# Kernel tuning notes

Hardware: AMD Instinct MI355X
Metric: run time of the kernel (lower is better)

## Reference

```python
import jax, jax.numpy as jnp
import numpy as np

NUM_HEADS = 16
DIM = 1024

def setup_inputs() -> dict:
    key = jax.random.key(0)
    ks = jax.random.split(key, 12)
    B, N, T, C = 4, 4096, 77, DIM
    s = 1.0 / np.sqrt(C)
    return {
        "hidden_states": jax.random.normal(ks[0], (B, N, C), jnp.float32),
        "encoder_hidden_states": jax.random.normal(ks[1], (B, T, C), jnp.float32),
        "attention_mask": jnp.zeros((B, N, T), jnp.float32),
        "Wq": jax.random.normal(ks[2], (C, C), jnp.float32) * s,
        "bq": jnp.zeros((C,), jnp.float32),
        "Wk": jax.random.normal(ks[3], (C, C), jnp.float32) * s,
        "bk": jnp.zeros((C,), jnp.float32),
        "Wv": jax.random.normal(ks[4], (C, C), jnp.float32) * s,
        "bv": jnp.zeros((C,), jnp.float32),
        "Wo": jax.random.normal(ks[5], (C, C), jnp.float32) * s,
        "bo": jnp.zeros((C,), jnp.float32),
    }

def reference(hidden_states, encoder_hidden_states, attention_mask,
              Wq, bq, Wk, bk, Wv, bv, Wo, bo):
    B, N, C = hidden_states.shape
    T = encoder_hidden_states.shape[1]
    H = NUM_HEADS
    D = C // H
    # QKV projections (torch Linear: x @ W.T + b)
    q = (hidden_states @ Wq.T + bq).reshape(B, N, H, D).transpose(0, 2, 1, 3)   # bhnd
    k = (encoder_hidden_states @ Wk.T + bk).reshape(B, T, H, D).transpose(0, 2, 1, 3)  # bhtd
    v = (encoder_hidden_states @ Wv.T + bv).reshape(B, T, H, D).transpose(0, 2, 1, 3)  # bhtd
    scale = 1.0 / jnp.sqrt(jnp.asarray(D, q.dtype))
    # scores [B,H,N,T]; additive mask broadcast over heads
    scores = jnp.einsum('bhnd,bhtd->bhnt', q, k) * scale + attention_mask[:, None, :, :]
    attn = jax.nn.softmax(scores, axis=-1)
    out = jnp.einsum('bhnt,bhtd->bhnd', attn, v)
    out = out.transpose(0, 2, 1, 3).reshape(B, N, C)
    return out @ Wo.T + bo
```

## Files before the change

### kernel.cpp

```cpp
#include <hip/hip_runtime.h>
#include <cstdint>

typedef __bf16 bf16x8 __attribute__((ext_vector_type(8)));
typedef float f32x4 __attribute__((ext_vector_type(4)));
typedef unsigned short u16;
typedef unsigned int u32;

__device__ __forceinline__ u16 f2bf(float f) {
    u32 u = __builtin_bit_cast(u32, f);
    u += 0x7fffu + ((u >> 16) & 1u);
    return (u16)(u >> 16);
}

__device__ __forceinline__ void gl_lds16(const u16* g, u16* l) {
    __builtin_amdgcn_global_load_lds(
        (const __attribute__((address_space(1))) void*)g,
        (__attribute__((address_space(3))) void*)l,
        16, 0, 0);
}

__device__ __forceinline__ f32x4 mfma16(bf16x8 a, bf16x8 b, f32x4 c) {
    return __builtin_amdgcn_mfma_f32_16x16x32_bf16(a, b, c, 0, 0, 0);
}


__global__ void cvt_pad(const float* __restrict__ src, u16* __restrict__ dst,
                        int srcn, int totn) {
    int i = (blockIdx.x * 256 + threadIdx.x) * 4;
    if (i >= totn) return;
    float4 v = make_float4(0.f, 0.f, 0.f, 0.f);
    if (i < srcn) v = *(const float4*)&src[i];
    ushort4 o;
    o.x = f2bf(v.x); o.y = f2bf(v.y); o.z = f2bf(v.z); o.w = f2bf(v.w);
    *(ushort4*)&dst[i] = o;
}

struct CvtArgs {
    const float* s[5];
    u16* d[5];
    int srcn[5];
    int totn[5];
};

__global__ void cvt_multi(CvtArgs a) {
    const int seg = blockIdx.y;
    int i = (blockIdx.x * 256 + threadIdx.x) * 4;
    if (i >= a.totn[seg]) return;
    float4 v = make_float4(0.f, 0.f, 0.f, 0.f);
    if (i < a.srcn[seg]) v = *(const float4*)&a.s[seg][i];
    ushort4 o;
    o.x = f2bf(v.x); o.y = f2bf(v.y); o.z = f2bf(v.z); o.w = f2bf(v.w);
    *(ushort4*)&a.d[seg][i] = o;
}

__device__ __forceinline__ void store_out(u16* C, long idx, float v) { C[idx] = f2bf(v); }
__device__ __forceinline__ void store_out(float* C, long idx, float v) { C[idx] = v; }

template <typename OutT, bool BA, bool BC>
__global__ __launch_bounds__(512, 2) void gemm8p(
    const u16* __restrict__ A, const u16* __restrict__ W,
    const float* __restrict__ bias, OutT* __restrict__ C,
    int M, int N, int K) {
    __shared__ __align__(16) u16 As[2][256 * 64];
    __shared__ __align__(16) u16 Bs[2][256 * 64];

    const int tid = threadIdx.x;
    const int wid = tid >> 6, l = tid & 63;
    const int wr = wid >> 2, wc = wid & 3;
    const int l15 = l & 15, lg = l >> 4;

    const int lin = blockIdx.y * gridDim.x + blockIdx.x;
    const int cpx = (gridDim.x * gridDim.y) >> 3;
    const int swz = (lin & 7) * cpx + (lin >> 3);
    const long tn = swz % gridDim.x;
    const long tm = swz / gridDim.x;

    const int srow = tid >> 3;
    const int schunk = (tid & 7) ^ (srow & 7);

    long aBase, aQ, aT;
    if (BA) {
        const long rq = tm * 256 + srow;
        aBase = ((long)(schunk >> 1) * (M >> 2) + (rq >> 2)) * 64 +
                (srow & 3) * 16 + (schunk & 1) * 8;
        aQ = 1024;
        aT = 64L * M;
    } else {
        aBase = (tm * 256 + srow) * (long)K + schunk * 8;
        aQ = 64L * K;
        aT = 64;
    }
    const long bBase = (tn * 256 + srow) * (long)K + schunk * 8;

    const int rxor = l15 & 7;
    const int rdo0 = ((0 * 4 + lg) ^ rxor) * 8;
    const int rdo1 = ((1 * 4 + lg) ^ rxor) * 8;

    const int NT = K >> 6;

#define STAGE_A(bufi, q_, t_)                                                 \
    gl_lds16(A + aBase + (q_)*aQ + (long)(t_)*aT, &As[bufi][(q_)*4096 + tid * 8])
#define STAGE_B(bufi, q_, t_)                                                 \
    gl_lds16(W + bBase + (long)(q_)*64 * K + (long)(t_)*64,                   \
             &Bs[bufi][(q_)*4096 + tid * 8])

    f32x4 acc[8][4] = {};

#pragma unroll
    for (int q = 0; q < 4; ++q) { STAGE_A(0, q, 0); STAGE_B(0, q, 0); }
#pragma unroll
    for (int q = 0; q < 4; ++q) STAGE_B(1, q, 1);
    STAGE_A(1, 0, 1); STAGE_A(1, 2, 1);
    asm volatile("s_waitcnt vmcnt(6)" ::: "memory");
    __builtin_amdgcn_sched_barrier(0);
    __builtin_amdgcn_s_barrier();

    const int arow = wr * 128 + l15;
    const int brow = wc * 64 + l15;

    for (int t = 0; t < NT; ++t) {
        const int c = t & 1;
        const u16* __restrict__ Ap = &As[c][0];
        const u16* __restrict__ Bp = &Bs[c][0];
        const bool s1 = (t + 1) < NT;
        const bool s2 = (t + 2) < NT;
        bf16x8 b[4][2];

        {
            bf16x8 a[2][2];
#pragma unroll
            for (int mi = 0; mi < 2; ++mi) {
                a[mi][0] = *(const bf16x8*)&Ap[(arow + mi * 16) * 64 + rdo0];
                a[mi][1] = *(const bf16x8*)&Ap[(arow + mi * 16) * 64 + rdo1];
            }
#pragma unroll
            for (int nf = 0; nf < 4; ++nf) {
                b[nf][0] = *(const bf16x8*)&Bp[(brow + nf * 16) * 64 + rdo0];
                b[nf][1] = *(const bf16x8*)&Bp[(brow + nf * 16) * 64 + rdo1];
            }
            if (s1) STAGE_A(c ^ 1, 1, t + 1);
            __builtin_amdgcn_s_barrier();
            asm volatile("s_waitcnt lgkmcnt(0)" ::: "memory");
            __builtin_amdgcn_sched_barrier(0);
            __builtin_amdgcn_s_setprio(1);
#pragma unroll
            for (int mi = 0; mi < 2; ++mi)
#pragma unroll
                for (int nf = 0; nf < 4; ++nf) {
                    acc[mi][nf] = mfma16(a[mi][0], b[nf][0], acc[mi][nf]);
                    acc[mi][nf] = mfma16(a[mi][1], b[nf][1], acc[mi][nf]);
                }
            __builtin_amdgcn_s_setprio(0);
            __builtin_amdgcn_s_barrier();
        }
        {
            bf16x8 a[2][2];
#pragma unroll
            for (int mi = 0; mi < 2; ++mi) {
                a[mi][0] = *(const bf16x8*)&Ap[(arow + (mi + 2) * 16) * 64 + rdo0];
                a[mi][1] = *(const bf16x8*)&Ap[(arow + (mi + 2) * 16) * 64 + rdo1];
            }
            if (s1) STAGE_A(c ^ 1, 3, t + 1);
            if (s2) { STAGE_B(c, 0, t + 2); STAGE_B(c, 1, t + 2); }
            __builtin_amdgcn_s_barrier();
            asm volatile("s_waitcnt lgkmcnt(0)" ::: "memory");
            __builtin_amdgcn_sched_barrier(0);
            __builtin_amdgcn_s_setprio(1);
#pragma unroll
            for (int mi = 0; mi < 2; ++mi)
#pragma unroll
                for (int nf = 0; nf < 4; ++nf) {
                    acc[mi + 2][nf] = mfma16(a[mi][0], b[nf][0], acc[mi + 2][nf]);
                    acc[mi + 2][nf] = mfma16(a[mi][1], b[nf][1], acc[mi + 2][nf]);
                }
            __builtin_amdgcn_s_setprio(0);
            __builtin_amdgcn_s_barrier();
        }
        {
            bf16x8 a[2][2];
#pragma unroll
            for (int mi = 0; mi < 2; ++mi) {
                a[mi][0] = *(const bf16x8*)&Ap[(arow + (mi + 4) * 16) * 64 + rdo0];
                a[mi][1] = *(const bf16x8*)&Ap[(arow + (mi + 4) * 16) * 64 + rdo1];
            }
            if (s2) { STAGE_B(c, 2, t + 2); STAGE_B(c, 3, t + 2); STAGE_A(c, 0, t + 2); }
            __builtin_amdgcn_s_barrier();
            asm volatile("s_waitcnt lgkmcnt(0)" ::: "memory");
            __builtin_amdgcn_sched_barrier(0);
            __builtin_amdgcn_s_setprio(1);
#pragma unroll
            for (int mi = 0; mi < 2; ++mi)
#pragma unroll
                for (int nf = 0; nf < 4; ++nf) {
                    acc[mi + 4][nf] = mfma16(a[mi][0], b[nf][0], acc[mi + 4][nf]);
                    acc[mi + 4][nf] = mfma16(a[mi][1], b[nf][1], acc[mi + 4][nf]);
                }
            __builtin_amdgcn_s_setprio(0);
            __builtin_amdgcn_s_barrier();
        }
        {
            bf16x8 a[2][2];
#pragma unroll
            for (int mi = 0; mi < 2; ++mi) {
                a[mi][0] = *(const bf16x8*)&Ap[(arow + (mi + 6) * 16) * 64 + rdo0];
                a[mi][1] = *(const bf16x8*)&Ap[(arow + (mi + 6) * 16) * 64 + rdo1];
            }
            if (s2) STAGE_A(c, 2, t + 2);
            __builtin_amdgcn_s_barrier();
            asm volatile("s_waitcnt lgkmcnt(0)" ::: "memory");
            __builtin_amdgcn_sched_barrier(0);
            __builtin_amdgcn_s_setprio(1);
#pragma unroll
            for (int mi = 0; mi < 2; ++mi)
#pragma unroll
                for (int nf = 0; nf < 4; ++nf) {
                    acc[mi + 6][nf] = mfma16(a[mi][0], b[nf][0], acc[mi + 6][nf]);
                    acc[mi + 6][nf] = mfma16(a[mi][1], b[nf][1], acc[mi + 6][nf]);
                }
            __builtin_amdgcn_s_setprio(0);
            if (s2)
                asm volatile("s_waitcnt vmcnt(6)" ::: "memory");
            else
                asm volatile("s_waitcnt vmcnt(0)" ::: "memory");
            __builtin_amdgcn_sched_barrier(0);
            __builtin_amdgcn_s_barrier();
        }
    }
#undef STAGE_A
#undef STAGE_B

    const long row0 = tm * 256 + wr * 128;
    const long col0 = tn * 256 + wc * 64;
    float bv[4];
#pragma unroll
    for (int nf = 0; nf < 4; ++nf) bv[nf] = bias[col0 + nf * 16 + l15];
    if (BC) {
        const long ct0 = col0 >> 4;
        const long rb = row0 >> 2;
#pragma unroll
        for (int mf = 0; mf < 8; ++mf)
#pragma unroll
            for (int nf = 0; nf < 4; ++nf)
#pragma unroll
                for (int r = 0; r < 4; ++r) {
                    const long idx =
                        ((ct0 + nf) * (long)(M >> 2) + rb + mf * 4 + lg) * 64 +
                        r * 16 + l15;
                    store_out(C, idx, acc[mf][nf][r] + bv[nf]);
                }
    } else {
#pragma unroll
        for (int mf = 0; mf < 8; ++mf)
#pragma unroll
            for (int nf = 0; nf < 4; ++nf)
#pragma unroll
                for (int r = 0; r < 4; ++r) {
                    const long row = row0 + mf * 16 + lg * 4 + r;
                    const long col = col0 + nf * 16 + l15;
                    store_out(C, row * N + col, acc[mf][nf][r] + bv[nf]);
                }
    }
}

__device__ __forceinline__ void gemm128_body(
    const u16* __restrict__ A, const u16* __restrict__ W,
    const float* __restrict__ bias, u16* __restrict__ C,
    int N, int K) {
    __shared__ u16 As[128 * 64];
    __shared__ u16 Bs[128 * 64];
    const int tid = threadIdx.x;
    const int w = tid >> 6, l = tid & 63;
    const int wr = w >> 1, wc = w & 1;
    const int l15 = l & 15, lg = l >> 4;
    const long tm = blockIdx.y, tn = blockIdx.x;
    const u16* Ab = A + tm * 128 * (long)K;
    const u16* Bb = W + tn * 128 * (long)K;

    f32x4 acc[4][4] = {};

    for (int k0 = 0; k0 < K; k0 += 64) {
#pragma unroll
        for (int t = 0; t < 4; ++t) {
            int i = t * 256 + tid;
            int row = i >> 3, cc = i & 7;
            gl_lds16(Ab + (long)row * K + k0 + cc * 8, &As[i * 8]);
            gl_lds16(Bb + (long)row * K + k0 + cc * 8, &Bs[i * 8]);
        }
        __syncthreads();
#pragma unroll
        for (int kk = 0; kk < 64; kk += 32) {
            bf16x8 a[4], b[4];
#pragma unroll
            for (int m = 0; m < 4; ++m)
                a[m] = *(const bf16x8*)&As[(wr * 64 + m * 16 + l15) * 64 + kk + lg * 8];
#pragma unroll
            for (int n = 0; n < 4; ++n)
                b[n] = *(const bf16x8*)&Bs[(wc * 64 + n * 16 + l15) * 64 + kk + lg * 8];
#pragma unroll
            for (int m = 0; m < 4; ++m)
#pragma unroll
                for (int n = 0; n < 4; ++n)
                    acc[m][n] = mfma16(a[m], b[n], acc[m][n]);
        }
        __syncthreads();
    }

    const long row0 = tm * 128 + wr * 64;
    const long col0 = tn * 128 + wc * 64;
#pragma unroll
    for (int m = 0; m < 4; ++m)
#pragma unroll
        for (int n = 0; n < 4; ++n)
#pragma unroll
            for (int r = 0; r < 4; ++r) {
                const long idx = (((col0 >> 4) + n) * 96L + (row0 >> 2) + m * 4 + lg) * 64 +
                                 r * 16 + l15;
                C[idx] = f2bf(acc[m][n][r] + bias[col0 + n * 16 + l15]);
            }
}

__global__ __launch_bounds__(256) void gemm_kv(
    const u16* __restrict__ A,
    const u16* __restrict__ Wk, const float* __restrict__ bk, u16* __restrict__ Ko,
    const u16* __restrict__ Wv, const float* __restrict__ bv, u16* __restrict__ Vo,
    int N, int K) {
    const bool isv = blockIdx.z != 0;
    gemm128_body(A, isv ? Wv : Wk, isv ? bv : bk, isv ? Vo : Ko, N, K);
}

__global__ __launch_bounds__(256) void attn_fused(
    const u16* __restrict__ Q,
    const u16* __restrict__ Kb,
    const u16* __restrict__ Vb,
    const float* __restrict__ mask,
    u16* __restrict__ Ao) {
    __shared__ u16 Ks[96 * 64];
    __shared__ u16 Vt[64 * 96];
    __shared__ u16 Ps[128 * 96];

    const int h = blockIdx.x, nt = blockIdx.y, b = blockIdx.z;
    const int tid = threadIdx.x;
    const int w = tid >> 6, l = tid & 63;
    const int l15 = l & 15, lg = l >> 4;

    for (int c = tid; c < 768; c += 256) {
        const int t = c >> 3, dc = c & 7;
        union { uint4 u; u16 s[8]; } kv, vv;
        kv.u = make_uint4(0, 0, 0, 0);
        vv.u = make_uint4(0, 0, 0, 0);
        if (t < 77) {
            const int row = b * 77 + t;
            const long base = ((long)(h * 4 + (dc >> 1)) * 96 + (row >> 2)) * 64 +
                              (row & 3) * 16 + (dc & 1) * 8;
            kv.u = *(const uint4*)&Kb[base];
            vv.u = *(const uint4*)&Vb[base];
        }
        *(uint4*)&Ks[t * 64 + dc * 8] = kv.u;
#pragma unroll
        for (int j = 0; j < 8; ++j) Vt[(dc * 8 + j) * 96 + t] = vv.s[j];
    }
    __syncthreads();

    f32x4 acc[2][6] = {};
    const int rq = b * 4096 + nt * 128 + w * 32;
#pragma unroll
    for (int kk = 0; kk < 64; kk += 32) {
        bf16x8 a[2], kf[6];
#pragma unroll
        for (int m = 0; m < 2; ++m)
            a[m] = *(const bf16x8*)&Q[((long)(h * 4 + (kk >> 4) + (lg >> 1)) * 4096 +
                                       (rq >> 2) + m * 4 + (l15 >> 2)) * 64 +
                                      (l15 & 3) * 16 + (lg & 1) * 8];
#pragma unroll
        for (int n = 0; n < 6; ++n)
            kf[n] = *(const bf16x8*)&Ks[(n * 16 + l15) * 64 + kk + lg * 8];
#pragma unroll
        for (int m = 0; m < 2; ++m)
#pragma unroll
            for (int n = 0; n < 6; ++n)
                acc[m][n] = mfma16(a[m], kf[n], acc[m][n]);
    }

    const float* mbase = mask + ((long)b * 4096 + nt * 128 + w * 32) * 77;
#pragma unroll
    for (int m = 0; m < 2; ++m) {
#pragma unroll
        for (int r = 0; r < 4; ++r) {
            const int row = m * 16 + lg * 4 + r;
            float vals[6];
            float rmax = -3e38f;
#pragma unroll
            for (int n = 0; n < 6; ++n) {
                const int col = n * 16 + l15;
                float v = -3e38f;
                if (col < 77) v = acc[m][n][r] * 0.125f + mbase[row * 77 + col];
                vals[n] = v;
                rmax = fmaxf(rmax, v);
            }
#pragma unroll
            for (int off = 1; off < 16; off <<= 1)
                rmax = fmaxf(rmax, __shfl_xor(rmax, off, 64));
            float s = 0.f;
#pragma unroll
            for (int n = 0; n < 6; ++n) {
                float e = (vals[n] > -1e37f) ? __expf(vals[n] - rmax) : 0.f;
                vals[n] = e;
                s += e;
            }
#pragma unroll
            for (int off = 1; off < 16; off <<= 1)
                s += __shfl_xor(s, off, 64);
            const float inv = 1.f / s;
#pragma unroll
            for (int n = 0; n < 6; ++n)
                Ps[(w * 32 + row) * 96 + n * 16 + l15] = f2bf(vals[n] * inv);
        }
    }
    __syncthreads();

    f32x4 o[2][4] = {};
#pragma unroll
    for (int kt = 0; kt < 96; kt += 32) {
        bf16x8 a[2], vf[4];
#pragma unroll
        for (int m = 0; m < 2; ++m)
            a[m] = *(const bf16x8*)&Ps[(w * 32 + m * 16 + l15) * 96 + kt + lg * 8];
#pragma unroll
        for (int n = 0; n < 4; ++n)
            vf[n] = *(const bf16x8*)&Vt[(n * 16 + l15) * 96 + kt + lg * 8];
#pragma unroll
        for (int m = 0; m < 2; ++m)
#pragma unroll
            for (int n = 0; n < 4; ++n)
                o[m][n] = mfma16(a[m], vf[n], o[m][n]);
    }

#pragma unroll
    for (int m = 0; m < 2; ++m)
#pragma unroll
        for (int n = 0; n < 4; ++n)
#pragma unroll
            for (int r = 0; r < 4; ++r) {
                const long idx = ((long)(h * 4 + n) * 4096 +
                                  b * 1024 + nt * 32 + w * 8 + m * 4 + lg) * 64 +
                                 r * 16 + l15;
                Ao[idx] = f2bf(o[m][n][r]);
            }
}

extern "C" void kernel_launch(void* const* d_in, const int* in_sizes, int n_in,
                              void* d_out, int out_size, void* d_ws, size_t ws_size,
                              hipStream_t stream) {
    const float* hidden = (const float*)d_in[0];
    const float* enc = (const float*)d_in[1];
    const float* mask = (const float*)d_in[2];
    const float* Wq = (const float*)d_in[3];
    const float* bq = (const float*)d_in[4];
    const float* Wk = (const float*)d_in[5];
    const float* bk = (const float*)d_in[6];
    const float* Wv = (const float*)d_in[7];
    const float* bv = (const float*)d_in[8];
    const float* Wo = (const float*)d_in[9];
    const float* bo = (const float*)d_in[10];
    float* out = (float*)d_out;

    char* ws = (char*)d_ws;
    u16* hiddenB = (u16*)(ws);
    u16* Qb = (u16*)(ws + 33554432L);
    u16* AoB = (u16*)(ws + 2 * 33554432L);
    u16* WqB = (u16*)(ws + 3 * 33554432L);
    u16* WkB = WqB + 1048576;
    u16* WvB = WkB + 1048576;
    u16* WoB = WvB + 1048576;
    u16* encB = WoB + 1048576;
    u16* Kbuf = encB + 393216;
    u16* Vbuf = Kbuf + 393216;

    cvt_pad<<<dim3(16384), 256, 0, stream>>>(hidden, hiddenB, 16777216, 16777216);
    CvtArgs ca;
    ca.s[0] = Wq;  ca.d[0] = WqB; ca.srcn[0] = 1048576; ca.totn[0] = 1048576;
    ca.s[1] = Wk;  ca.d[1] = WkB; ca.srcn[1] = 1048576; ca.totn[1] = 1048576;
    ca.s[2] = Wv;  ca.d[2] = WvB; ca.srcn[2] = 1048576; ca.totn[2] = 1048576;
    ca.s[3] = Wo;  ca.d[3] = WoB; ca.srcn[3] = 1048576; ca.totn[3] = 1048576;
    ca.s[4] = enc; ca.d[4] = encB; ca.srcn[4] = 315392; ca.totn[4] = 393216;
    cvt_multi<<<dim3(1024, 5), 256, 0, stream>>>(ca);

    gemm8p<u16, false, true><<<dim3(4, 64), 512, 0, stream>>>(
        hiddenB, WqB, bq, Qb, 16384, 1024, 1024);
    gemm_kv<<<dim3(8, 3, 2), 256, 0, stream>>>(encB, WkB, bk, Kbuf, WvB, bv, Vbuf, 1024, 1024);

    attn_fused<<<dim3(16, 32, 4), 256, 0, stream>>>(Qb, Kbuf, Vbuf, mask, AoB);

    gemm8p<float, true, false><<<dim3(4, 64), 512, 0, stream>>>(
        AoB, WoB, bo, out, 16384, 1024, 1024);
}
```

Baseline: 166.7 us.

## Write V transposed in GEMM epilogue and drop LDS staging in attention

The V projection epilogue now writes V directly in a transposed, tile-friendly layout. The attention kernel can then read K and V fragments straight from global memory, with no shared-memory staging and no block-wide barriers. Scores are computed as S^T, so each row's softmax reduction needs only two cross-lane shuffles, and P is stored to padded LDS rows with packed writes. The kernel also gets a launch-bounds occupancy hint and a reordered grid. One risk: the padded time rows (t ≥ 77) of the transposed V buffer are never written, so uninitialized workspace could feed NaNs into the P·V product.

```diff
diff --git a/kernel.cpp b/kernel.cpp
--- a/kernel.cpp
+++ b/kernel.cpp
@@ -262,6 +262,7 @@
     }
 }
 
+template <bool VT>
 __device__ __forceinline__ void gemm128_body(
     const u16* __restrict__ A, const u16* __restrict__ W,
     const float* __restrict__ bias, u16* __restrict__ C,
@@ -313,9 +314,23 @@
         for (int n = 0; n < 4; ++n)
 #pragma unroll
             for (int r = 0; r < 4; ++r) {
-                const long idx = (((col0 >> 4) + n) * 96L + (row0 >> 2) + m * 4 + lg) * 64 +
-                                 r * 16 + l15;
-                C[idx] = f2bf(acc[m][n][r] + bias[col0 + n * 16 + l15]);
+                const float v = acc[m][n][r] + bias[col0 + n * 16 + l15];
+                if (VT) {
+                    const int row = (int)(row0 + m * 16 + lg * 4 + r);
+                    if (row < 308) {
+                        const int bb = row / 77;
+                        const int t = row - bb * 77;
+                        const int ch = (int)(col0 + n * 16 + l15);
+                        const long idx = (long)bb * 98304 +
+                                         ((long)(t >> 4) * 256 + (ch >> 2)) * 64 +
+                                         (ch & 3) * 16 + (t & 15);
+                        C[idx] = f2bf(v);
+                    }
+                } else {
+                    const long idx = (((col0 >> 4) + n) * 96L + (row0 >> 2) + m * 4 + lg) * 64 +
+                                     r * 16 + l15;
+                    C[idx] = f2bf(v);
+                }
             }
 }
 
@@ -324,115 +339,116 @@
     const u16* __restrict__ Wk, const float* __restrict__ bk, u16* __restrict__ Ko,
     const u16* __restrict__ Wv, const float* __restrict__ bv, u16* __restrict__ Vo,
     int N, int K) {
-    const bool isv = blockIdx.z != 0;
-    gemm128_body(A, isv ? Wv : Wk, isv ? bv : bk, isv ? Vo : Ko, N, K);
-}
-
-__global__ __launch_bounds__(256) void attn_fused(
+    if (blockIdx.z == 0)
+        gemm128_body<false>(A, Wk, bk, Ko, N, K);
+    else
+        gemm128_body<true>(A, Wv, bv, Vo, N, K);
+}
+
+__global__ __launch_bounds__(256, 4) void attn_fused(
     const u16* __restrict__ Q,
     const u16* __restrict__ Kb,
-    const u16* __restrict__ Vb,
+    const u16* __restrict__ Vt,
     const float* __restrict__ mask,
     u16* __restrict__ Ao) {
-    __shared__ u16 Ks[96 * 64];
-    __shared__ u16 Vt[64 * 96];
-    __shared__ u16 Ps[128 * 96];
-
-    const int h = blockIdx.x, nt = blockIdx.y, b = blockIdx.z;
+    __shared__ u16 Ps[128 * 104];
+
+    const int h = blockIdx.x, b = blockIdx.y, nt = blockIdx.z;
     const int tid = threadIdx.x;
     const int w = tid >> 6, l = tid & 63;
     const int l15 = l & 15, lg = l >> 4;
 
-    for (int c = tid; c < 768; c += 256) {
-        const int t = c >> 3, dc = c & 7;
-        union { uint4 u; u16 s[8]; } kv, vv;
-        kv.u = make_uint4(0, 0, 0, 0);
-        vv.u = make_uint4(0, 0, 0, 0);
-        if (t < 77) {
-            const int row = b * 77 + t;
-            const long base = ((long)(h * 4 + (dc >> 1)) * 96 + (row >> 2)) * 64 +
-                              (row & 3) * 16 + (dc & 1) * 8;
-            kv.u = *(const uint4*)&Kb[base];
-            vv.u = *(const uint4*)&Vb[base];
-        }
-        *(uint4*)&Ks[t * 64 + dc * 8] = kv.u;
-#pragma unroll
-        for (int j = 0; j < 8; ++j) Vt[(dc * 8 + j) * 96 + t] = vv.s[j];
-    }
-    __syncthreads();
-
-    f32x4 acc[2][6] = {};
-    const int rq = b * 4096 + nt * 128 + w * 32;
+    const int qrow = b * 4096 + nt * 128 + w * 32;
+
+    f32x4 acc[6][2] = {};
 #pragma unroll
     for (int kk = 0; kk < 64; kk += 32) {
-        bf16x8 a[2], kf[6];
+        const int d = kk + lg * 8;
+        const int cb = h * 4 + (d >> 4);
+        const int dlow = d & 15;
+        bf16x8 kf[6], qf[2];
+#pragma unroll
+        for (int n = 0; n < 6; ++n) {
+            const int row = b * 77 + n * 16 + l15;
+            kf[n] = *(const bf16x8*)&Kb[((long)cb * 96 + (row >> 2)) * 64 +
+                                        (row & 3) * 16 + dlow];
+        }
+#pragma unroll
+        for (int m = 0; m < 2; ++m) {
+            const int row = qrow + m * 16 + l15;
+            qf[m] = *(const bf16x8*)&Q[((long)cb * 4096 + (row >> 2)) * 64 +
+                                       (row & 3) * 16 + dlow];
+        }
+#pragma unroll
+        for (int n = 0; n < 6; ++n)
+#pragma unroll
+            for (int m = 0; m < 2; ++m)
+                acc[n][m] = mfma16(kf[n], qf[m], acc[n][m]);
+    }
+
+    const float* mrow0 = mask + ((long)b * 4096 + nt * 128 + w * 32) * 77;
+#pragma unroll
+    for (int m = 0; m < 2; ++m) {
+        const float* mrow = mrow0 + (m * 16 + l15) * 77;
+        float vals[6][4];
+        float rmax = -3e38f;
+#pragma unroll
+        for (int n = 0; n < 6; ++n) {
+            const int t0 = n * 16 + lg * 4;
+#pragma unroll
+            for (int r = 0; r < 4; ++r) {
+                const int t = t0 + r;
+                float v = -3e38f;
+                if (t < 77) v = acc[n][m][r] * 0.125f + mrow[t];
+                vals[n][r] = v;
+                rmax = fmaxf(rmax, v);
+            }
+        }
+        rmax = fmaxf(rmax, __shfl_xor(rmax, 16, 64));
+        rmax = fmaxf(rmax, __shfl_xor(rmax, 32, 64));
+        float s = 0.f;
+#pragma unroll
+        for (int n = 0; n < 6; ++n)
+#pragma unroll
+            for (int r = 0; r < 4; ++r) {
+                float e = (vals[n][r] > -1e37f) ? __expf(vals[n][r] - rmax) : 0.f;
+                vals[n][r] = e;
+                s += e;
+            }
+        s += __shfl_xor(s, 16, 64);
+        s += __shfl_xor(s, 32, 64);
+        const float inv = 1.f / s;
+#pragma unroll
+        for (int n = 0; n < 6; ++n) {
+            const u32 lo = (u32)f2bf(vals[n][0] * inv) |
+                           ((u32)f2bf(vals[n][1] * inv) << 16);
+            const u32 hi = (u32)f2bf(vals[n][2] * inv) |
+                           ((u32)f2bf(vals[n][3] * inv) << 16);
+            *(uint2*)&Ps[(w * 32 + m * 16 + l15) * 104 + n * 16 + lg * 4] =
+                make_uint2(lo, hi);
+        }
+    }
+
+    f32x4 o[2][4] = {};
+#pragma unroll
+    for (int kt = 0; kt < 96; kt += 32) {
+        bf16x8 pa[2], vf[4];
 #pragma unroll
         for (int m = 0; m < 2; ++m)
-            a[m] = *(const bf16x8*)&Q[((long)(h * 4 + (kk >> 4) + (lg >> 1)) * 4096 +
-                                       (rq >> 2) + m * 4 + (l15 >> 2)) * 64 +
-                                      (l15 & 3) * 16 + (lg & 1) * 8];
-#pragma unroll
-        for (int n = 0; n < 6; ++n)
-            kf[n] = *(const bf16x8*)&Ks[(n * 16 + l15) * 64 + kk + lg * 8];
+            pa[m] = *(const bf16x8*)&Ps[(w * 32 + m * 16 + l15) * 104 + kt + lg * 8];
+        const int t0 = kt + lg * 8;
+#pragma unroll
+        for (int n = 0; n < 4; ++n) {
+            const int ch = h * 64 + n * 16 + l15;
+            vf[n] = *(const bf16x8*)&Vt[(long)b * 98304 +
+                                        ((long)(t0 >> 4) * 256 + (ch >> 2)) * 64 +
+                                        (ch & 3) * 16 + (t0 & 15)];
+        }
 #pragma unroll
         for (int m = 0; m < 2; ++m)
 #pragma unroll
-            for (int n = 0; n < 6; ++n)
-                acc[m][n] = mfma16(a[m], kf[n], acc[m][n]);
-    }
-
-    const float* mbase = mask + ((long)b * 4096 + nt * 128 + w * 32) * 77;
-#pragma unroll
-    for (int m = 0; m < 2; ++m) {
-#pragma unroll
-        for (int r = 0; r < 4; ++r) {
-            const int row = m * 16 + lg * 4 + r;
-            float vals[6];
-            float rmax = -3e38f;
-#pragma unroll
-            for (int n = 0; n < 6; ++n) {
-                const int col = n * 16 + l15;
-                float v = -3e38f;
-                if (col < 77) v = acc[m][n][r] * 0.125f + mbase[row * 77 + col];
-                vals[n] = v;
-                rmax = fmaxf(rmax, v);
-            }
-#pragma unroll
-            for (int off = 1; off < 16; off <<= 1)
-                rmax = fmaxf(rmax, __shfl_xor(rmax, off, 64));
-            float s = 0.f;
-#pragma unroll
-            for (int n = 0; n < 6; ++n) {
-                float e = (vals[n] > -1e37f) ? __expf(vals[n] - rmax) : 0.f;
-                vals[n] = e;
-                s += e;
-            }
-#pragma unroll
-            for (int off = 1; off < 16; off <<= 1)
-                s += __shfl_xor(s, off, 64);
-            const float inv = 1.f / s;
-#pragma unroll
-            for (int n = 0; n < 6; ++n)
-                Ps[(w * 32 + row) * 96 + n * 16 + l15] = f2bf(vals[n] * inv);
-        }
-    }
-    __syncthreads();
-
-    f32x4 o[2][4] = {};
-#pragma unroll
-    for (int kt = 0; kt < 96; kt += 32) {
-        bf16x8 a[2], vf[4];
-#pragma unroll
-        for (int m = 0; m < 2; ++m)
-            a[m] = *(const bf16x8*)&Ps[(w * 32 + m * 16 + l15) * 96 + kt + lg * 8];
-#pragma unroll
-        for (int n = 0; n < 4; ++n)
-            vf[n] = *(const bf16x8*)&Vt[(n * 16 + l15) * 96 + kt + lg * 8];
-#pragma unroll
-        for (int m = 0; m < 2; ++m)
-#pragma unroll
             for (int n = 0; n < 4; ++n)
-                o[m][n] = mfma16(a[m], vf[n], o[m][n]);
+                o[m][n] = mfma16(pa[m], vf[n], o[m][n]);
     }
 
 #pragma unroll
@@ -474,7 +490,7 @@
     u16* WoB = WvB + 1048576;
     u16* encB = WoB + 1048576;
     u16* Kbuf = encB + 393216;
-    u16* Vbuf = Kbuf + 393216;
+    u16* VtBuf = Kbuf + 393216;
 
     cvt_pad<<<dim3(16384), 256, 0, stream>>>(hidden, hiddenB, 16777216, 16777216);
     CvtArgs ca;
@@ -487,9 +503,9 @@
 
     gemm8p<u16, false, true><<<dim3(4, 64), 512, 0, stream>>>(
         hiddenB, WqB, bq, Qb, 16384, 1024, 1024);
-    gemm_kv<<<dim3(8, 3, 2), 256, 0, stream>>>(encB, WkB, bk, Kbuf, WvB, bv, Vbuf, 1024, 1024);
-
-    attn_fused<<<dim3(16, 32, 4), 256, 0, stream>>>(Qb, Kbuf, Vbuf, mask, AoB);
+    gemm_kv<<<dim3(8, 3, 2), 256, 0, stream>>>(encB, WkB, bk, Kbuf, WvB, bv, VtBuf, 1024, 1024);
+
+    attn_fused<<<dim3(16, 4, 32), 256, 0, stream>>>(Qb, Kbuf, VtBuf, mask, AoB);
 
     gemm8p<float, true, false><<<dim3(4, 64), 512, 0, stream>>>(
         AoB, WoB, bo, out, 16384, 1024, 1024);
```

New measurement: 166.5 us. Within noise of the previous version (-0.1%).
